# Kernel optimization log

Measured on AMD Instinct MI355X. Metric: run time of the kernel, lower is better.

## Reference

```python
import jax, jax.numpy as jnp
import numpy as np

THR = 0.6
EPS = 1e-12


def _mlp(x, w1, b1, w2, b2):
    # Linear -> ReLU -> (Dropout eval = identity) -> Linear
    return jax.nn.relu(x @ w1 + b1) @ w2 + b2


def setup_inputs() -> dict:
    B, H, D = 16384, 1024, 300
    key = jax.random.key(0)
    ks = jax.random.split(key, 32)
    s = 0.02
    inp = {
        'brics': jax.random.normal(ks[0], (B, H), jnp.float32),
        'function_group': jax.random.normal(ks[1], (B, H), jnp.float32),
        'pharmacophore': jax.random.normal(ks[2], (B, H), jnp.float32),
        # fingerprint encoders (brics / function_group / pharmacophore)
        'bw1': jax.random.normal(ks[3], (H, D), jnp.float32) * s,
        'bb1': jnp.zeros((D,), jnp.float32),
        'bw2': jax.random.normal(ks[4], (D, H), jnp.float32) * s,
        'bb2': jnp.zeros((H,), jnp.float32),
        'fw1': jax.random.normal(ks[5], (H, D), jnp.float32) * s,
        'fb1': jnp.zeros((D,), jnp.float32),
        'fw2': jax.random.normal(ks[6], (D, H), jnp.float32) * s,
        'fb2': jnp.zeros((H,), jnp.float32),
        'pw1': jax.random.normal(ks[7], (H, D), jnp.float32) * s,
        'pb1': jnp.zeros((D,), jnp.float32),
        'pw2': jax.random.normal(ks[8], (D, H), jnp.float32) * s,
        'pb2': jnp.zeros((H,), jnp.float32),
        # weight generator: Linear(3H, 3)
        'wg_W': jax.random.normal(ks[9], (3 * H, 3), jnp.float32) * s,
        'wg_b': jnp.zeros((3,), jnp.float32),
        # enhancement layer: Linear(H, H) + sigmoid
        'enh_W': jax.random.normal(ks[10], (H, H), jnp.float32) * s,
        'enh_b': jnp.zeros((H,), jnp.float32),
        # fusion layer: Linear(2H, H)
        'fus_W': jax.random.normal(ks[11], (2 * H, H), jnp.float32) * s,
        'fus_b': jnp.zeros((H,), jnp.float32),
    }
    return inp


def reference(brics, function_group, pharmacophore,
              bw1, bb1, bw2, bb2,
              fw1, fb1, fw2, fb2,
              pw1, pb1, pw2, pb2,
              wg_W, wg_b, enh_W, enh_b, fus_W, fus_b):
    B, H = brics.shape
    eb = _mlp(brics, bw1, bb1, bw2, bb2)            # [B,H]
    ef = _mlp(function_group, fw1, fb1, fw2, fb2)   # [B,H]
    ep = _mlp(pharmacophore, pw1, pb1, pw2, pb2)    # [B,H]

    E = jnp.stack([eb, ef, ep], axis=1)             # [B,3,H]
    En = E / jnp.maximum(jnp.linalg.norm(E, axis=-1, keepdims=True), EPS)

    # three unordered pairs (0,1),(0,2),(1,2); softmax-weighted sum is
    # permutation invariant, so the original python sort is a no-op.
    ii = jnp.array([0, 0, 1])
    jj = jnp.array([1, 2, 2])
    Ei, Ej = E[:, ii], E[:, jj]                     # [B,3,H]
    Eni, Enj = En[:, ii], En[:, jj]
    sim = jnp.sum(Eni * Enj, axis=-1)               # [B,3] cosine sims
    keep = sim > THR                                # pairs above threshold

    elem_mask = (Eni * Enj > THR).astype(E.dtype)   # [B,3,H]
    cf = 0.5 * (Ei + Ej) * elem_mask                # candidate common feats

    w = jax.nn.softmax(jnp.where(keep, sim, -1e9), axis=-1)  # [B,3]
    wsum = jnp.einsum('bp,bph->bh', w, cf)
    mean_fp = jnp.mean(E, axis=1)
    any_kept = jnp.any(keep, axis=-1, keepdims=True)
    common = jnp.where(any_kept, wsum, mean_fp)     # [B,H]

    all_cat = jnp.concatenate([eb, ef, ep], axis=1)          # [B,3H]
    fp_w = jax.nn.softmax(all_cat @ wg_W + wg_b, axis=1)     # [B,3]
    weighted_fp_sum = jnp.einsum('bk,bkh->bh', fp_w, E)

    enh = jax.nn.sigmoid(common @ enh_W + enh_b)
    enhanced_common = common * enh

    fused = jnp.concatenate([weighted_fp_sum, enhanced_common], axis=1) @ fus_W + fus_b
    return fused
```

## Files before the change

kernel.cpp:

```cpp
#include <hip/hip_runtime.h>
#include <stdint.h>


typedef __attribute__((ext_vector_type(8))) __bf16 bf16x8;
typedef __attribute__((ext_vector_type(8))) short short8;
typedef __attribute__((ext_vector_type(4))) float floatx4;

__device__ __forceinline__ uint16_t f2bf(float f) {
  __bf16 h = (__bf16)f;
  return __builtin_bit_cast(uint16_t, h);
}
__device__ __forceinline__ float bf2f(uint16_t h) {
  union { uint32_t u; float f; } v; v.u = ((uint32_t)h) << 16;
  return v.f;
}
__device__ __forceinline__ short8 pack8(float4 a, float4 b) {
  union { __bf16 h[8]; short8 s; } u;
  u.h[0] = (__bf16)a.x; u.h[1] = (__bf16)a.y; u.h[2] = (__bf16)a.z; u.h[3] = (__bf16)a.w;
  u.h[4] = (__bf16)b.x; u.h[5] = (__bf16)b.y; u.h[6] = (__bf16)b.z; u.h[7] = (__bf16)b.w;
  return u.s;
}
__device__ __forceinline__ void gload16(const void* g, void* l) {
  __builtin_amdgcn_global_load_lds(
      (const __attribute__((address_space(1))) void*)g,
      (__attribute__((address_space(3))) void*)l, 16, 0, 0);
}

__global__ void cfe_transpose_all(const float* __restrict__ bw1, const float* __restrict__ fw1,
                                  const float* __restrict__ pw1, const float* __restrict__ bw2,
                                  const float* __restrict__ fw2, const float* __restrict__ pw2,
                                  const float* __restrict__ enhW, const float* __restrict__ fusW,
                                  uint16_t* __restrict__ W1T, uint16_t* __restrict__ W2T,
                                  uint16_t* __restrict__ ENHT, uint16_t* __restrict__ FUST) {
  int bid = blockIdx.x;
  const float* src; uint16_t* dst; int K, N, Kpad, Npad, bx, by;
  if (bid < 1152) {
    int z = bid / 384, t = bid % 384; bx = t % 32; by = t / 32;
    src = (z == 0) ? bw1 : ((z == 1) ? fw1 : pw1); dst = W1T + (long)z * 384 * 1024;
    K = 1024; N = 300; Kpad = 1024; Npad = 384;
  } else if (bid < 2112) {
    bid -= 1152; int z = bid / 320, t = bid % 320; bx = t % 10; by = t / 10;
    src = (z == 0) ? bw2 : ((z == 1) ? fw2 : pw2); dst = W2T + (long)z * 1024 * 320;
    K = 300; N = 1024; Kpad = 320; Npad = 1024;
  } else if (bid < 3136) {
    bid -= 2112; bx = bid % 32; by = bid / 32;
    src = enhW; dst = ENHT; K = 1024; N = 1024; Kpad = 1024; Npad = 1024;
  } else {
    bid -= 3136; bx = bid % 64; by = bid / 64;
    src = fusW; dst = FUST; K = 2048; N = 1024; Kpad = 2048; Npad = 1024;
  }
  __shared__ float tile[32][33];
  const int tx = threadIdx.x & 31;
  const int ty = threadIdx.x >> 5;
  const int k0 = bx * 32;
  const int n0 = by * 32;
#pragma unroll
  for (int i = 0; i < 4; i++) {
    int k = k0 + ty + 8 * i;
    int n = n0 + tx;
    tile[ty + 8 * i][tx] = (k < K && n < N) ? src[(long)k * N + n] : 0.f;
  }
  __syncthreads();
#pragma unroll
  for (int i = 0; i < 4; i++) {
    int n = n0 + ty + 8 * i;
    int k = k0 + tx;
    if (n < Npad && k < Kpad) dst[(long)n * Kpad + k] = f2bf(tile[tx][ty + 8 * i]);
  }
}

template <int MODE, int AF32>
__global__ void cfe_gemm128(const void* __restrict__ A0, const void* __restrict__ A1,
                            const void* __restrict__ A2, int lda,
                            const uint16_t* __restrict__ Bt, long sBz, int ldb,
                            void* __restrict__ C, long sCz, int ldc, int colofs,
                            const float* __restrict__ bias0,
                            const float* __restrict__ bias1,
                            const float* __restrict__ bias2, int biasN,
                            const uint16_t* __restrict__ common, int K) {
  const int z = blockIdx.z;
  const void* Av = (z == 0) ? A0 : ((z == 1) ? A1 : A2);
  Bt += (long)z * sBz;
  const float* bias = (z == 0) ? bias0 : ((z == 1) ? bias1 : bias2);

  const int gx = gridDim.x;
  const int lin = blockIdx.y * gx + blockIdx.x;
  const int P = (gx * gridDim.y) >> 3;
  const int v = (lin & 7) * P + (lin >> 3);
  const long bm = (long)(v / gx) * 128;
  const long bn = (long)(v % gx) * 128;

  const int tid = threadIdx.x;
  const int wave = tid >> 6;
  const int lane = tid & 63;
  const int wm = wave >> 1;
  const int wn = wave & 1;

  constexpr int ASZ16 = AF32 ? 128 * 64 : 128 * 32;
  constexpr int BSZ16 = 128 * 32;
  __shared__ __attribute__((aligned(16))) uint16_t As[2 * ASZ16];
  __shared__ __attribute__((aligned(16))) uint16_t Bs[2 * BSZ16];

  floatx4 acc[4][4];
#pragma unroll
  for (int i = 0; i < 4; i++)
#pragma unroll
    for (int j = 0; j < 4; j++) acc[i][j] = (floatx4){0.f, 0.f, 0.f, 0.f};

  const int lrow = lane >> 2;
  const int lcolB = (((lane & 3) ^ ((lrow >> 1) & 3)) * 8);
  const uint16_t* Bp = Bt + (bn + wave * 32 + lrow) * (long)ldb + lcolB;
  const uint16_t* Ap = nullptr;
  if constexpr (!AF32) {
    Ap = (const uint16_t*)Av + (bm + wave * 32 + lrow) * (long)lda + lcolB;
  }

  const float* ApS = nullptr;
  if constexpr (AF32) {
    const int r_in = lane >> 3;
    const int gpos = (lane & 7) >> 1;
    const int halfp = lane & 1;
    const int scol = ((gpos ^ (r_in & 3)) << 3) | ((halfp ^ ((r_in >> 2) & 1)) << 2);
    ApS = (const float*)Av + (bm + wave * 32 + r_in) * (long)lda + scol;
  }

  auto stage = [&](int k0, int p) {
    if constexpr (AF32) {
      char* AsBp = (char*)As + p * (ASZ16 * 2) + (wave * 32) * 128;
      gload16(ApS + k0, AsBp);
      gload16(ApS + 8 * (long)lda + k0, AsBp + 1024);
      gload16(ApS + 16 * (long)lda + k0, AsBp + 2048);
      gload16(ApS + 24 * (long)lda + k0, AsBp + 3072);
    } else {
      uint16_t* AsP = As + p * ASZ16 + (wave * 32) * 32;
      gload16(Ap + k0, AsP);
      gload16(Ap + 16 * (long)lda + k0, AsP + 16 * 32);
    }
    uint16_t* BsP = Bs + p * BSZ16 + (wave * 32) * 32;
    gload16(Bp + k0, BsP);
    gload16(Bp + 16 * (long)ldb + k0, BsP + 16 * 32);
  };

  const int fr = lane & 15;
  const int fq = lane >> 4;
  const int swr = (fr >> 1) & 3;
  const uint16_t* ArBase = &As[(wm * 64 + fr) * 32 + (fq ^ swr) * 8];
  const uint16_t* BrBase = &Bs[(wn * 64 + fr) * 32 + (fq ^ swr) * 8];
  const int ga = fq ^ (fr & 3);
  const int hb = (fr >> 2) & 1;
  const float* AfBase = (const float*)As + (wm * 64 + fr) * 32 + ga * 8;

  auto compute_tile = [&](int p) {
    short8 a[4], b[4];
    if constexpr (AF32) {
      const float* Af = AfBase + p * (ASZ16 / 2);
#pragma unroll
      for (int mi = 0; mi < 4; mi++) {
        const float* Afm = Af + mi * 512;
        float4 lo = *(const float4*)(Afm + hb * 4);
        float4 hi = *(const float4*)(Afm + (hb ^ 1) * 4);
        a[mi] = pack8(lo, hi);
      }
    } else {
      const uint16_t* Ar = ArBase + p * ASZ16;
#pragma unroll
      for (int mi = 0; mi < 4; mi++) a[mi] = *(const short8*)(Ar + mi * 512);
    }
    const uint16_t* Br = BrBase + p * BSZ16;
#pragma unroll
    for (int ni = 0; ni < 4; ni++) b[ni] = *(const short8*)(Br + ni * 512);
#pragma unroll
    for (int mi = 0; mi < 4; mi++)
#pragma unroll
      for (int ni = 0; ni < 4; ni++)
        acc[mi][ni] = __builtin_amdgcn_mfma_f32_16x16x32_bf16(
            __builtin_bit_cast(bf16x8, a[mi]), __builtin_bit_cast(bf16x8, b[ni]),
            acc[mi][ni], 0, 0, 0);
  };

  const int nt = K >> 5;
  int pb = 0;
  stage(0, 0);
  for (int t = 0; t + 1 < nt; ++t, pb ^= 1) {
    stage((t + 1) << 5, pb ^ 1);
    if constexpr (AF32) {
      asm volatile("s_waitcnt vmcnt(6)" ::: "memory");
    } else {
      asm volatile("s_waitcnt vmcnt(4)" ::: "memory");
    }
    __builtin_amdgcn_s_barrier();
    __builtin_amdgcn_sched_barrier(0);
    compute_tile(pb);
    __builtin_amdgcn_sched_barrier(0);
    __builtin_amdgcn_s_barrier();
  }
  asm volatile("s_waitcnt vmcnt(0)" ::: "memory");
  __builtin_amdgcn_s_barrier();
  __builtin_amdgcn_sched_barrier(0);
  compute_tile(pb);

#pragma unroll
  for (int mi = 0; mi < 4; mi++) {
    long row = bm + wm * 64 + mi * 16 + fq * 4;
#pragma unroll
    for (int ni = 0; ni < 4; ni++) {
      long col = bn + wn * 64 + ni * 16 + fr;
      float bv = (col < biasN) ? bias[col] : 0.f;
#pragma unroll
      for (int r = 0; r < 4; r++) {
        float vv = acc[mi][ni][r] + bv;
        long idx = (row + r) * (long)ldc + colofs + col;
        if constexpr (MODE == 0) {
          ((uint16_t*)C)[(long)z * sCz + idx] = f2bf(fmaxf(vv, 0.f));
        } else if constexpr (MODE == 1) {
          ((uint16_t*)C)[(long)z * sCz + idx] = f2bf(vv);
        } else if constexpr (MODE == 2) {
          float c = bf2f(common[(row + r) * 1024 + col]);
          float s = 1.f / (1.f + __expf(-vv));
          ((uint16_t*)C)[idx] = f2bf(c * s);
        } else {
          ((float*)C)[idx] = vv;
        }
      }
    }
  }
}

__global__ void cfe_pointwise_kernel(const uint16_t* __restrict__ E,
                                     const float* __restrict__ wgW,
                                     const float* __restrict__ wgb,
                                     uint16_t* __restrict__ commonb,
                                     uint16_t* __restrict__ fusedA) {
  const int row = blockIdx.x;
  const int tid = threadIdx.x;
  const long ES = 16384L * 1024;
  const long base = (long)row * 1024 + tid * 4;

  ushort4 u0 = *(const ushort4*)(E + base);
  ushort4 u1 = *(const ushort4*)(E + ES + base);
  ushort4 u2 = *(const ushort4*)(E + 2 * ES + base);
  float eb[4] = {bf2f(u0.x), bf2f(u0.y), bf2f(u0.z), bf2f(u0.w)};
  float ef[4] = {bf2f(u1.x), bf2f(u1.y), bf2f(u1.z), bf2f(u1.w)};
  float ep[4] = {bf2f(u2.x), bf2f(u2.y), bf2f(u2.z), bf2f(u2.w)};

  float vals[9];
#pragma unroll
  for (int i = 0; i < 9; i++) vals[i] = 0.f;
#pragma unroll
  for (int j = 0; j < 4; j++) {
    int h = tid * 4 + j;
    vals[0] += eb[j] * eb[j];
    vals[1] += ef[j] * ef[j];
    vals[2] += ep[j] * ep[j];
    vals[3] += eb[j] * ef[j];
    vals[4] += eb[j] * ep[j];
    vals[5] += ef[j] * ep[j];
#pragma unroll
    for (int c = 0; c < 3; c++)
      vals[6 + c] += eb[j] * wgW[(long)h * 3 + c] +
                     ef[j] * wgW[(long)(1024 + h) * 3 + c] +
                     ep[j] * wgW[(long)(2048 + h) * 3 + c];
  }

#pragma unroll
  for (int i = 0; i < 9; i++) {
    float v = vals[i];
    for (int off = 32; off; off >>= 1) v += __shfl_down(v, off);
    vals[i] = v;
  }
  __shared__ float red[4][9];
  if ((tid & 63) == 0) {
#pragma unroll
    for (int i = 0; i < 9; i++) red[tid >> 6][i] = vals[i];
  }
  __syncthreads();
  float tot[9];
#pragma unroll
  for (int i = 0; i < 9; i++)
    tot[i] = red[0][i] + red[1][i] + red[2][i] + red[3][i];

  const float EPSF = 1e-12f;
  float nb = fmaxf(sqrtf(tot[0]), EPSF);
  float nf = fmaxf(sqrtf(tot[1]), EPSF);
  float np_ = fmaxf(sqrtf(tot[2]), EPSF);
  float s01 = tot[3] / (nb * nf);
  float s02 = tot[4] / (nb * np_);
  float s12 = tot[5] / (nf * np_);
  bool k01 = s01 > 0.6f, k02 = s02 > 0.6f, k12 = s12 > 0.6f;
  bool any = k01 | k02 | k12;
  float z0 = k01 ? s01 : -1e9f;
  float z1 = k02 ? s02 : -1e9f;
  float z2 = k12 ? s12 : -1e9f;
  float zm = fmaxf(z0, fmaxf(z1, z2));
  float w0 = __expf(z0 - zm), w1 = __expf(z1 - zm), w2 = __expf(z2 - zm);
  float wsum = w0 + w1 + w2;
  w0 /= wsum; w1 /= wsum; w2 /= wsum;

  float g0 = tot[6] + wgb[0], g1 = tot[7] + wgb[1], g2 = tot[8] + wgb[2];
  float gm = fmaxf(g0, fmaxf(g1, g2));
  float f0 = __expf(g0 - gm), f1 = __expf(g1 - gm), f2 = __expf(g2 - gm);
  float fs = f0 + f1 + f2;
  f0 /= fs; f1 /= fs; f2 /= fs;

  float inb = 1.f / nb, inf_ = 1.f / nf, inp = 1.f / np_;
  ushort4 co, wf;
  uint16_t cov[4], wfv[4];
#pragma unroll
  for (int j = 0; j < 4; j++) {
    float b = eb[j], f = ef[j], p = ep[j];
    float nbv = b * inb, nfv = f * inf_, npv = p * inp;
    float c01 = (nbv * nfv > 0.6f) ? 0.5f * (b + f) : 0.f;
    float c02 = (nbv * npv > 0.6f) ? 0.5f * (b + p) : 0.f;
    float c12 = (nfv * npv > 0.6f) ? 0.5f * (f + p) : 0.f;
    float ws = w0 * c01 + w1 * c02 + w2 * c12;
    float cm = any ? ws : (b + f + p) * (1.f / 3.f);
    float wfs = f0 * b + f1 * f + f2 * p;
    cov[j] = f2bf(cm);
    wfv[j] = f2bf(wfs);
  }
  co.x = cov[0]; co.y = cov[1]; co.z = cov[2]; co.w = cov[3];
  wf.x = wfv[0]; wf.y = wfv[1]; wf.z = wfv[2]; wf.w = wfv[3];
  *(ushort4*)(commonb + base) = co;
  *(ushort4*)(fusedA + (long)row * 2048 + tid * 4) = wf;
}

extern "C" void kernel_launch(void* const* d_in, const int* in_sizes, int n_in,
                              void* d_out, int out_size, void* d_ws, size_t ws_size,
                              hipStream_t stream) {
  (void)in_sizes; (void)n_in; (void)out_size; (void)ws_size;
  const float* brics = (const float*)d_in[0];
  const float* fg    = (const float*)d_in[1];
  const float* ph    = (const float*)d_in[2];
  const float* bw1 = (const float*)d_in[3];  const float* bb1 = (const float*)d_in[4];
  const float* bw2 = (const float*)d_in[5];  const float* bb2 = (const float*)d_in[6];
  const float* fw1 = (const float*)d_in[7];  const float* fb1 = (const float*)d_in[8];
  const float* fw2 = (const float*)d_in[9];  const float* fb2 = (const float*)d_in[10];
  const float* pw1 = (const float*)d_in[11]; const float* pb1 = (const float*)d_in[12];
  const float* pw2 = (const float*)d_in[13]; const float* pb2 = (const float*)d_in[14];
  const float* wgW = (const float*)d_in[15]; const float* wgb = (const float*)d_in[16];
  const float* enhW = (const float*)d_in[17]; const float* enhb = (const float*)d_in[18];
  const float* fusW = (const float*)d_in[19]; const float* fusb = (const float*)d_in[20];
  float* out = (float*)d_out;

  uint16_t* EB   = (uint16_t*)d_ws;
  uint16_t* FA   = EB + 3L * 16384 * 1024;
  uint16_t* W1T  = FA + 16384L * 2048;
  uint16_t* W2T  = W1T + 3L * 384 * 1024;
  uint16_t* ENHT = W2T + 3L * 1024 * 320;
  uint16_t* FUST = ENHT + 1024L * 1024;
  uint16_t* YB   = (uint16_t*)d_out;
  uint16_t* COM  = (uint16_t*)d_out;

  cfe_transpose_all<<<5184, 256, 0, stream>>>(
      bw1, fw1, pw1, bw2, fw2, pw2, enhW, fusW, W1T, W2T, ENHT, FUST);

  cfe_gemm128<0, 1><<<dim3(3, 128, 3), 256, 0, stream>>>(
      brics, fg, ph, 1024, W1T, 384L * 1024, 1024,
      YB, 16384L * 384, 384, 0, bb1, fb1, pb1, 300, nullptr, 1024);

  cfe_gemm128<1, 0><<<dim3(8, 128, 3), 256, 0, stream>>>(
      YB, YB + 16384L * 384, YB + 2 * 16384L * 384, 384, W2T, 1024L * 320, 320,
      EB, 16384L * 1024, 1024, 0, bb2, fb2, pb2, 1024, nullptr, 320);

  cfe_pointwise_kernel<<<16384, 256, 0, stream>>>(EB, wgW, wgb, COM, FA);

  cfe_gemm128<2, 0><<<dim3(8, 128, 1), 256, 0, stream>>>(
      COM, COM, COM, 1024, ENHT, 0, 1024,
      FA, 0, 2048, 1024, enhb, enhb, enhb, 1024, COM, 1024);

  cfe_gemm128<3, 0><<<dim3(8, 128, 1), 256, 0, stream>>>(
      FA, FA, FA, 2048, FUST, 0, 2048,
      out, 0, 1024, 0, fusb, fusb, fusb, 1024, nullptr, 2048);
}
```

Before: 545.9 us.

## Generalize GEMM to larger 512-thread tiles with triple-buffered LDS pipeline

Templates the GEMM on block tile sizes and moves to 8 waves per block, using 128x384 tiles for the first encoder layer and 256x256 tiles for the other GEMMs. LDS staging goes from double to triple buffering, issuing loads two K-steps ahead with adjusted vmcnt waits. Larger tiles raise operand reuse per global load and cut redundant A reads. The cost is more LDS and registers per block, lower occupancy, and fewer blocks per wave of the grid.

```diff
diff --git a/kernel.cpp b/kernel.cpp
--- a/kernel.cpp
+++ b/kernel.cpp
@@ -69,15 +69,23 @@
   }
 }
 
-template <int MODE, int AF32>
-__global__ void cfe_gemm128(const void* __restrict__ A0, const void* __restrict__ A1,
-                            const void* __restrict__ A2, int lda,
-                            const uint16_t* __restrict__ Bt, long sBz, int ldb,
-                            void* __restrict__ C, long sCz, int ldc, int colofs,
-                            const float* __restrict__ bias0,
-                            const float* __restrict__ bias1,
-                            const float* __restrict__ bias2, int biasN,
-                            const uint16_t* __restrict__ common, int K) {
+template <int MODE, int AF32, int BM, int BN>
+__global__ __launch_bounds__(512, 2) void cfe_gemm(
+    const void* __restrict__ A0, const void* __restrict__ A1,
+    const void* __restrict__ A2, int lda,
+    const uint16_t* __restrict__ Bt, long sBz, int ldb,
+    void* __restrict__ C, long sCz, int ldc, int colofs,
+    const float* __restrict__ bias0, const float* __restrict__ bias1,
+    const float* __restrict__ bias2, int biasN,
+    const uint16_t* __restrict__ common, int K) {
+  constexpr int MR = BM / 32;
+  constexpr int NR = BN / 64;
+  constexpr int ASZ = AF32 ? BM * 64 : BM * 32;
+  constexpr int BSZ = BN * 32;
+  constexpr int NA_I = AF32 ? BM / 64 : BM / 128;
+  constexpr int NB_I = BN / 128;
+  constexpr int LPT = NA_I + NB_I;
+
   const int z = blockIdx.z;
   const void* Av = (z == 0) ? A0 : ((z == 1) ? A1 : A2);
   Bt += (long)z * sBz;
@@ -87,32 +95,30 @@
   const int lin = blockIdx.y * gx + blockIdx.x;
   const int P = (gx * gridDim.y) >> 3;
   const int v = (lin & 7) * P + (lin >> 3);
-  const long bm = (long)(v / gx) * 128;
-  const long bn = (long)(v % gx) * 128;
+  const long bm = (long)(v / gx) * BM;
+  const long bn = (long)(v % gx) * BN;
 
   const int tid = threadIdx.x;
   const int wave = tid >> 6;
   const int lane = tid & 63;
-  const int wm = wave >> 1;
-  const int wn = wave & 1;
-
-  constexpr int ASZ16 = AF32 ? 128 * 64 : 128 * 32;
-  constexpr int BSZ16 = 128 * 32;
-  __shared__ __attribute__((aligned(16))) uint16_t As[2 * ASZ16];
-  __shared__ __attribute__((aligned(16))) uint16_t Bs[2 * BSZ16];
-
-  floatx4 acc[4][4];
-#pragma unroll
-  for (int i = 0; i < 4; i++)
-#pragma unroll
-    for (int j = 0; j < 4; j++) acc[i][j] = (floatx4){0.f, 0.f, 0.f, 0.f};
+  const int wm = wave >> 2;
+  const int wn = wave & 3;
+
+  __shared__ __attribute__((aligned(16))) uint16_t As[3 * ASZ];
+  __shared__ __attribute__((aligned(16))) uint16_t Bs[3 * BSZ];
+
+  floatx4 acc[MR][NR];
+#pragma unroll
+  for (int i = 0; i < MR; i++)
+#pragma unroll
+    for (int j = 0; j < NR; j++) acc[i][j] = (floatx4){0.f, 0.f, 0.f, 0.f};
 
   const int lrow = lane >> 2;
   const int lcolB = (((lane & 3) ^ ((lrow >> 1) & 3)) * 8);
-  const uint16_t* Bp = Bt + (bn + wave * 32 + lrow) * (long)ldb + lcolB;
+  const uint16_t* Bp = Bt + (bn + wave * (BN / 8) + lrow) * (long)ldb + lcolB;
   const uint16_t* Ap = nullptr;
   if constexpr (!AF32) {
-    Ap = (const uint16_t*)Av + (bm + wave * 32 + lrow) * (long)lda + lcolB;
+    Ap = (const uint16_t*)Av + (bm + wave * (BM / 8) + lrow) * (long)lda + lcolB;
   }
 
   const float* ApS = nullptr;
@@ -121,90 +127,94 @@
     const int gpos = (lane & 7) >> 1;
     const int halfp = lane & 1;
     const int scol = ((gpos ^ (r_in & 3)) << 3) | ((halfp ^ ((r_in >> 2) & 1)) << 2);
-    ApS = (const float*)Av + (bm + wave * 32 + r_in) * (long)lda + scol;
+    ApS = (const float*)Av + (bm + wave * (BM / 8) + r_in) * (long)lda + scol;
   }
 
   auto stage = [&](int k0, int p) {
     if constexpr (AF32) {
-      char* AsBp = (char*)As + p * (ASZ16 * 2) + (wave * 32) * 128;
-      gload16(ApS + k0, AsBp);
-      gload16(ApS + 8 * (long)lda + k0, AsBp + 1024);
-      gload16(ApS + 16 * (long)lda + k0, AsBp + 2048);
-      gload16(ApS + 24 * (long)lda + k0, AsBp + 3072);
+      char* AsBp = (char*)As + p * (ASZ * 2) + wave * (BM / 8) * 128;
+#pragma unroll
+      for (int i = 0; i < NA_I; i++)
+        gload16(ApS + (long)(8 * i) * lda + k0, AsBp + i * 1024);
     } else {
-      uint16_t* AsP = As + p * ASZ16 + (wave * 32) * 32;
-      gload16(Ap + k0, AsP);
-      gload16(Ap + 16 * (long)lda + k0, AsP + 16 * 32);
+      uint16_t* AsP = As + p * ASZ + wave * (BM / 8) * 32;
+#pragma unroll
+      for (int i = 0; i < NA_I; i++)
+        gload16(Ap + (long)(16 * i) * lda + k0, AsP + i * 16 * 32);
     }
-    uint16_t* BsP = Bs + p * BSZ16 + (wave * 32) * 32;
-    gload16(Bp + k0, BsP);
-    gload16(Bp + 16 * (long)ldb + k0, BsP + 16 * 32);
+    uint16_t* BsP = Bs + p * BSZ + wave * (BN / 8) * 32;
+#pragma unroll
+    for (int i = 0; i < NB_I; i++)
+      gload16(Bp + (long)(16 * i) * ldb + k0, BsP + i * 16 * 32);
   };
 
   const int fr = lane & 15;
   const int fq = lane >> 4;
   const int swr = (fr >> 1) & 3;
-  const uint16_t* ArBase = &As[(wm * 64 + fr) * 32 + (fq ^ swr) * 8];
-  const uint16_t* BrBase = &Bs[(wn * 64 + fr) * 32 + (fq ^ swr) * 8];
+  const uint16_t* ArBase = &As[(wm * (MR * 16) + fr) * 32 + (fq ^ swr) * 8];
+  const uint16_t* BrBase = &Bs[(wn * (NR * 16) + fr) * 32 + (fq ^ swr) * 8];
   const int ga = fq ^ (fr & 3);
   const int hb = (fr >> 2) & 1;
-  const float* AfBase = (const float*)As + (wm * 64 + fr) * 32 + ga * 8;
+  const float* AfBase = (const float*)As + (wm * (MR * 16) + fr) * 32 + ga * 8;
 
   auto compute_tile = [&](int p) {
-    short8 a[4], b[4];
+    short8 a[MR], b[NR];
     if constexpr (AF32) {
-      const float* Af = AfBase + p * (ASZ16 / 2);
-#pragma unroll
-      for (int mi = 0; mi < 4; mi++) {
+      const float* Af = AfBase + p * (ASZ / 2);
+#pragma unroll
+      for (int mi = 0; mi < MR; mi++) {
         const float* Afm = Af + mi * 512;
         float4 lo = *(const float4*)(Afm + hb * 4);
         float4 hi = *(const float4*)(Afm + (hb ^ 1) * 4);
         a[mi] = pack8(lo, hi);
       }
     } else {
-      const uint16_t* Ar = ArBase + p * ASZ16;
-#pragma unroll
-      for (int mi = 0; mi < 4; mi++) a[mi] = *(const short8*)(Ar + mi * 512);
+      const uint16_t* Ar = ArBase + p * ASZ;
+#pragma unroll
+      for (int mi = 0; mi < MR; mi++) a[mi] = *(const short8*)(Ar + mi * 512);
     }
-    const uint16_t* Br = BrBase + p * BSZ16;
-#pragma unroll
-    for (int ni = 0; ni < 4; ni++) b[ni] = *(const short8*)(Br + ni * 512);
-#pragma unroll
-    for (int mi = 0; mi < 4; mi++)
-#pragma unroll
-      for (int ni = 0; ni < 4; ni++)
+    const uint16_t* Br = BrBase + p * BSZ;
+#pragma unroll
+    for (int ni = 0; ni < NR; ni++) b[ni] = *(const short8*)(Br + ni * 512);
+#pragma unroll
+    for (int mi = 0; mi < MR; mi++)
+#pragma unroll
+      for (int ni = 0; ni < NR; ni++)
         acc[mi][ni] = __builtin_amdgcn_mfma_f32_16x16x32_bf16(
             __builtin_bit_cast(bf16x8, a[mi]), __builtin_bit_cast(bf16x8, b[ni]),
             acc[mi][ni], 0, 0, 0);
   };
 
   const int nt = K >> 5;
+  stage(0, 0);
+  stage(32, 1);
   int pb = 0;
-  stage(0, 0);
-  for (int t = 0; t + 1 < nt; ++t, pb ^= 1) {
-    stage((t + 1) << 5, pb ^ 1);
-    if constexpr (AF32) {
-      asm volatile("s_waitcnt vmcnt(6)" ::: "memory");
+  for (int t = 0; t < nt; ++t) {
+    if (t + 2 < nt) {
+      int pt = pb + 2; if (pt >= 3) pt -= 3;
+      stage((t + 2) << 5, pt);
+      if constexpr (LPT == 5) asm volatile("s_waitcnt vmcnt(10)" ::: "memory");
+      else                    asm volatile("s_waitcnt vmcnt(8)"  ::: "memory");
+    } else if (t + 1 < nt) {
+      if constexpr (LPT == 5) asm volatile("s_waitcnt vmcnt(5)" ::: "memory");
+      else                    asm volatile("s_waitcnt vmcnt(4)" ::: "memory");
     } else {
-      asm volatile("s_waitcnt vmcnt(4)" ::: "memory");
+      asm volatile("s_waitcnt vmcnt(0)" ::: "memory");
     }
     __builtin_amdgcn_s_barrier();
     __builtin_amdgcn_sched_barrier(0);
     compute_tile(pb);
     __builtin_amdgcn_sched_barrier(0);
     __builtin_amdgcn_s_barrier();
-  }
-  asm volatile("s_waitcnt vmcnt(0)" ::: "memory");
-  __builtin_amdgcn_s_barrier();
-  __builtin_amdgcn_sched_barrier(0);
-  compute_tile(pb);
-
-#pragma unroll
-  for (int mi = 0; mi < 4; mi++) {
-    long row = bm + wm * 64 + mi * 16 + fq * 4;
-#pragma unroll
-    for (int ni = 0; ni < 4; ni++) {
-      long col = bn + wn * 64 + ni * 16 + fr;
+    pb += 1; if (pb == 3) pb = 0;
+  }
+
+#pragma unroll
+  for (int mi = 0; mi < MR; mi++) {
+    long row = bm + wm * (MR * 16) + mi * 16 + fq * 4;
+#pragma unroll
+    for (int ni = 0; ni < NR; ni++) {
+      long col = bn + wn * (NR * 16) + ni * 16 + fr;
       float bv = (col < biasN) ? bias[col] : 0.f;
 #pragma unroll
       for (int r = 0; r < 4; r++) {
@@ -354,21 +364,21 @@
   cfe_transpose_all<<<5184, 256, 0, stream>>>(
       bw1, fw1, pw1, bw2, fw2, pw2, enhW, fusW, W1T, W2T, ENHT, FUST);
 
-  cfe_gemm128<0, 1><<<dim3(3, 128, 3), 256, 0, stream>>>(
+  cfe_gemm<0, 1, 128, 384><<<dim3(1, 128, 3), 512, 0, stream>>>(
       brics, fg, ph, 1024, W1T, 384L * 1024, 1024,
       YB, 16384L * 384, 384, 0, bb1, fb1, pb1, 300, nullptr, 1024);
 
-  cfe_gemm128<1, 0><<<dim3(8, 128, 3), 256, 0, stream>>>(
+  cfe_gemm<1, 0, 256, 256><<<dim3(4, 64, 3), 512, 0, stream>>>(
       YB, YB + 16384L * 384, YB + 2 * 16384L * 384, 384, W2T, 1024L * 320, 320,
       EB, 16384L * 1024, 1024, 0, bb2, fb2, pb2, 1024, nullptr, 320);
 
   cfe_pointwise_kernel<<<16384, 256, 0, stream>>>(EB, wgW, wgb, COM, FA);
 
-  cfe_gemm128<2, 0><<<dim3(8, 128, 1), 256, 0, stream>>>(
+  cfe_gemm<2, 0, 256, 256><<<dim3(4, 64, 1), 512, 0, stream>>>(
       COM, COM, COM, 1024, ENHT, 0, 1024,
       FA, 0, 2048, 1024, enhb, enhb, enhb, 1024, COM, 1024);
 
-  cfe_gemm128<3, 0><<<dim3(8, 128, 1), 256, 0, stream>>>(
+  cfe_gemm<3, 0, 256, 256><<<dim3(4, 64, 1), 512, 0, stream>>>(
       FA, FA, FA, 2048, FUST, 0, 2048,
       out, 0, 1024, 0, fusb, fusb, fusb, 1024, nullptr, 2048);
 }
```

Result: slower. 604.3 us (+10.7%).

## Replace first MLP GEMM with full-N row-strip kernel reading fp32 input once

Applied to the files above, without the earlier changes.

Adds a dedicated kernel for the first encoder layer. Each block loads a 32-row strip of the fp32 input once, converts it to bf16 into swizzled LDS, and has 8 waves each compute 48 of the 384 output columns, reading the transposed weights directly from global memory. The old 128-tile GEMM re-read each input row tile across 3 N-tiles. This targets redundant fp32 activation traffic in a memory-bound layer, at the cost of un-staged global weight loads and a 64KB LDS footprint that limits occupancy.

```diff
diff --git a/kernel.cpp b/kernel.cpp
--- a/kernel.cpp
+++ b/kernel.cpp
@@ -69,6 +69,88 @@
   }
 }
 
+__global__ __launch_bounds__(512, 2) void cfe_gemm1(
+    const float* __restrict__ A0, const float* __restrict__ A1,
+    const float* __restrict__ A2,
+    const uint16_t* __restrict__ Bt,
+    uint16_t* __restrict__ C,
+    const float* __restrict__ bias0, const float* __restrict__ bias1,
+    const float* __restrict__ bias2) {
+  const int z = blockIdx.z;
+  const float* Av = (z == 0) ? A0 : ((z == 1) ? A1 : A2);
+  const uint16_t* B = Bt + (long)z * 384 * 1024;
+  const float* bias = (z == 0) ? bias0 : ((z == 1) ? bias1 : bias2);
+
+  const int lin = blockIdx.y;
+  const int v = (lin & 7) * 64 + (lin >> 3);
+  const long bm = (long)v * 32;
+
+  const int tid = threadIdx.x;
+  const int wave = tid >> 6;
+  const int lane = tid & 63;
+
+  __shared__ __attribute__((aligned(16))) uint16_t As[32 * 1024];
+
+#pragma unroll
+  for (int r_loc = 0; r_loc < 4; r_loc++) {
+    const int r = wave * 4 + r_loc;
+    const float* Arow = Av + (bm + r) * 1024L;
+#pragma unroll
+    for (int p = 0; p < 2; p++) {
+      const int lg = p * 64 + lane;
+      float4 f0 = *(const float4*)(Arow + lg * 8);
+      float4 f1 = *(const float4*)(Arow + lg * 8 + 4);
+      *(short8*)(As + r * 1024 + ((lg ^ (r & 7)) * 8)) = pack8(f0, f1);
+    }
+  }
+  __syncthreads();
+
+  const int fr = lane & 15;
+  const int fq = lane >> 4;
+
+  floatx4 acc[2][3];
+#pragma unroll
+  for (int i = 0; i < 2; i++)
+#pragma unroll
+    for (int j = 0; j < 3; j++) acc[i][j] = (floatx4){0.f, 0.f, 0.f, 0.f};
+
+  for (int kt = 0; kt < 32; kt++) {
+    short8 a[2], b[3];
+#pragma unroll
+    for (int mi = 0; mi < 2; mi++) {
+      const int row = mi * 16 + fr;
+      const int lg = kt * 4 + fq;
+      a[mi] = *(const short8*)(As + row * 1024 + ((lg ^ (row & 7)) * 8));
+    }
+#pragma unroll
+    for (int ni = 0; ni < 3; ni++)
+      b[ni] = *(const short8*)(B + (long)(wave * 48 + ni * 16 + fr) * 1024 +
+                               kt * 32 + fq * 8);
+#pragma unroll
+    for (int mi = 0; mi < 2; mi++)
+#pragma unroll
+      for (int ni = 0; ni < 3; ni++)
+        acc[mi][ni] = __builtin_amdgcn_mfma_f32_16x16x32_bf16(
+            __builtin_bit_cast(bf16x8, a[mi]), __builtin_bit_cast(bf16x8, b[ni]),
+            acc[mi][ni], 0, 0, 0);
+  }
+
+#pragma unroll
+  for (int mi = 0; mi < 2; mi++) {
+    long row = bm + mi * 16 + fq * 4;
+#pragma unroll
+    for (int ni = 0; ni < 3; ni++) {
+      int col = wave * 48 + ni * 16 + fr;
+      float bv = (col < 300) ? bias[col] : 0.f;
+#pragma unroll
+      for (int r = 0; r < 4; r++) {
+        float vv = acc[mi][ni][r] + bv;
+        C[(long)z * 16384 * 384 + (row + r) * 384 + col] = f2bf(fmaxf(vv, 0.f));
+      }
+    }
+  }
+}
+
 template <int MODE, int AF32>
 __global__ void cfe_gemm128(const void* __restrict__ A0, const void* __restrict__ A1,
                             const void* __restrict__ A2, int lda,
@@ -354,9 +436,8 @@
   cfe_transpose_all<<<5184, 256, 0, stream>>>(
       bw1, fw1, pw1, bw2, fw2, pw2, enhW, fusW, W1T, W2T, ENHT, FUST);
 
-  cfe_gemm128<0, 1><<<dim3(3, 128, 3), 256, 0, stream>>>(
-      brics, fg, ph, 1024, W1T, 384L * 1024, 1024,
-      YB, 16384L * 384, 384, 0, bb1, fb1, pb1, 300, nullptr, 1024);
+  cfe_gemm1<<<dim3(1, 512, 3), 512, 0, stream>>>(
+      brics, fg, ph, W1T, YB, bb1, fb1, pb1);
 
   cfe_gemm128<1, 0><<<dim3(8, 128, 3), 256, 0, stream>>>(
       YB, YB + 16384L * 384, YB + 2 * 16384L * 384, 384, W2T, 1024L * 320, 320,
```

After: 604.7 us. 1.11x slower.
